# Performance work log

Measured on AMD Instinct MI355X. Metric: run time of the kernel, lower is better.

The kernel has to match this reference:

```python
import jax, jax.numpy as jnp
import numpy as np

N = 100000  # nodes
E = 1600000  # edges


def gcn_conv(x, W, b, src, dst, n_nodes):
    """PyG-style GCNConv: add self-loops, symmetric norm, linear, scatter-add, bias."""
    h = x @ W  # [N, F_out]
    loop = jnp.arange(n_nodes, dtype=src.dtype)
    s = jnp.concatenate([src, loop])  # source nodes (messages flow src -> dst)
    d = jnp.concatenate([dst, loop])
    deg = jax.ops.segment_sum(jnp.ones_like(d, dtype=h.dtype), d, num_segments=n_nodes)
    dinv = jnp.where(deg > 0, jax.lax.rsqrt(deg), 0.0)
    norm = dinv[s] * dinv[d]  # [E+N]
    msgs = h[s] * norm[:, None]  # [E+N, F_out] -- dominant memory traffic
    out = jax.ops.segment_sum(msgs, d, num_segments=n_nodes)
    return out + b


def setup_inputs() -> dict:
    key = jax.random.key(0)
    k1, k2, k3, k4 = jax.random.split(key, 4)
    x = jax.random.normal(k1, (N, 128), dtype=jnp.float32)
    edge_index = jax.random.randint(k2, (2, E), 0, N, dtype=jnp.int32)
    W1 = jax.random.normal(k3, (128, 64), dtype=jnp.float32) * (1.0 / np.sqrt(128))
    b1 = jnp.zeros((64,), dtype=jnp.float32)
    W2 = jax.random.normal(k4, (64, 16), dtype=jnp.float32) * (1.0 / np.sqrt(64))
    b2 = jnp.zeros((16,), dtype=jnp.float32)
    return {"x": x, "edge_index": edge_index, "W1": W1, "b1": b1, "W2": W2, "b2": b2}


def reference(x, edge_index, W1, b1, W2, b2):
    src, dst = edge_index[0], edge_index[1]
    h = gcn_conv(x, W1, b1, src, dst, N)
    h = jax.nn.leaky_relu(h, negative_slope=0.2)
    # dropout is identity in eval mode
    h = gcn_conv(h, W2, b2, src, dst, N)
    return jax.nn.log_softmax(h, axis=-1)
```

## Files before the change

### kernel.cpp

```cpp
#include <hip/hip_runtime.h>
#include <math.h>


#define CHUNK 4096
#define BSHIFT 9
#define BMASK 511
#define CAP 9216

typedef __bf16 bf16x8 __attribute__((ext_vector_type(8)));
typedef float f32x4 __attribute__((ext_vector_type(4)));

__device__ __forceinline__ unsigned f2b(float f) {
  unsigned u = __float_as_uint(f);
  return (u + 0x7FFF + ((u >> 16) & 1)) >> 16;
}

__global__ void binit_kernel(int* __restrict__ gbcursor, int nbc,
                             unsigned* __restrict__ h1s, int n) {
  int b = blockIdx.x * 256 + threadIdx.x;
  if (b < nbc) gbcursor[b] = b * CAP;
  if (blockIdx.x == 0 && threadIdx.x < 32) h1s[(size_t)n * 32 + threadIdx.x] = 0u;
}

__global__ __launch_bounds__(256) void scatterA_kernel(const int* __restrict__ src,
                                                       const int* __restrict__ dst,
                                                       int E, int nbc,
                                                       int* __restrict__ gbcursor,
                                                       int* __restrict__ tmp) {
  __shared__ int hist[256];
  __shared__ int segcur[256];
  int tid = threadIdx.x;
  int estart = blockIdx.x * CHUNK;
  int eend = min(E, estart + CHUNK);
  hist[tid] = 0;
  __syncthreads();
  for (int i = estart + tid; i < eend; i += 256)
    atomicAdd(&hist[dst[i] >> BSHIFT], 1);
  __syncthreads();
  if (tid < nbc) {
    int c = hist[tid];
    segcur[tid] = c ? atomicAdd(&gbcursor[tid], c) : 0;
  }
  __syncthreads();
  for (int i = estart + tid; i < eend; i += 256) {
    int d = dst[i];
    int b = d >> BSHIFT;
    int pos = atomicAdd(&segcur[b], 1);
    if (pos < (b + 1) * CAP)
      tmp[pos] = (src[i] << BSHIFT) | (d & BMASK);
  }
}

__global__ __launch_bounds__(1024) void csrbuild_kernel(const int* __restrict__ tmp,
                                                        const int* __restrict__ gbcursor,
                                                        int n, int* __restrict__ row_start,
                                                        int* __restrict__ degs,
                                                        float* __restrict__ dinv,
                                                        int* __restrict__ csr) {
  __shared__ int nh[512];
  __shared__ int sc[512];
  __shared__ int lcur[512];
  int b = blockIdx.x, tid = threadIdx.x;
  int base = b * CAP;
  int count = min(gbcursor[b] - base, CAP);
  if (tid < 512) nh[tid] = 0;
  __syncthreads();
  for (int i = tid; i < count; i += 1024) atomicAdd(&nh[tmp[base + i] & BMASK], 1);
  __syncthreads();
  int d = 0;
  if (tid < 512) { d = nh[tid]; sc[tid] = d; }
  __syncthreads();
  for (int off = 1; off < 512; off <<= 1) {
    int a = 0;
    if (tid < 512) { a = sc[tid]; if (tid >= off) a += sc[tid - off]; }
    __syncthreads();
    if (tid < 512) sc[tid] = a;
    __syncthreads();
  }
  if (tid < 512) {
    int e0 = base + sc[tid] - d;
    lcur[tid] = e0;
    int v = (b << BSHIFT) + tid;
    if (v < n) {
      row_start[v] = e0; degs[v] = d;
      dinv[v] = rsqrtf((float)(d + 1));
    }
  }
  __syncthreads();
  for (int i = tid; i < count; i += 1024) {
    int val = tmp[base + i];
    int pos = atomicAdd(&lcur[val & BMASK], 1);
    csr[pos] = val >> BSHIFT;
  }
}

__global__ __launch_bounds__(256, 4) void gemm1_kernel(const float* __restrict__ x,
                                                       const float* __restrict__ W1,
                                                       const float* __restrict__ dinv,
                                                       unsigned* __restrict__ h1s, int n) {
  __shared__ unsigned lds_u[64 * 68 * 2];
  unsigned* xs = lds_u;
  unsigned* wt = lds_u + 64 * 68;
  int tid = threadIdx.x;
  int vb = blockIdx.x * 64;
  int nrows = min(64, n - vb);

  const float4* xg = (const float4*)(x + (size_t)vb * 128);
#pragma unroll
  for (int it = 0; it < 8; ++it) {
    int idx = it * 256 + tid;
    int r = idx >> 5, c2 = idx & 31;
    float4 vv = make_float4(0.f, 0.f, 0.f, 0.f);
    if (r < nrows) vv = xg[idx];
    xs[r * 68 + c2 * 2] = (f2b(vv.y) << 16) | f2b(vv.x);
    xs[r * 68 + c2 * 2 + 1] = (f2b(vv.w) << 16) | f2b(vv.z);
  }
  unsigned short* wt16 = (unsigned short*)wt;
  const float4* wg = (const float4*)W1;
#pragma unroll
  for (int it = 0; it < 8; ++it) {
    int idx = it * 256 + tid;
    int k = idx >> 4, n0 = (idx & 15) * 4;
    float4 wv = wg[idx];
    wt16[(n0 + 0) * 136 + k] = (unsigned short)f2b(wv.x);
    wt16[(n0 + 1) * 136 + k] = (unsigned short)f2b(wv.y);
    wt16[(n0 + 2) * 136 + k] = (unsigned short)f2b(wv.z);
    wt16[(n0 + 3) * 136 + k] = (unsigned short)f2b(wv.w);
  }
  __syncthreads();

  int lane = tid & 63, wid = tid >> 6;
  int m16 = lane & 15, quad = lane >> 4;
  const unsigned* xp = xs + (wid * 16 + m16) * 68 + quad * 4;
  const unsigned* wp = wt + m16 * 68 + quad * 4;
  f32x4 acc[4] = {};
#pragma unroll
  for (int ks = 0; ks < 4; ++ks) {
    bf16x8 a = *(const bf16x8*)(xp + ks * 16);
#pragma unroll
    for (int nt = 0; nt < 4; ++nt) {
      bf16x8 b = *(const bf16x8*)(wp + nt * 16 * 68 + ks * 16);
      acc[nt] = __builtin_amdgcn_mfma_f32_16x16x32_bf16(a, b, acc[nt], 0, 0, 0);
    }
  }
  int rbase = vb + wid * 16 + quad * 4;
  float dvv[4];
#pragma unroll
  for (int reg = 0; reg < 4; ++reg) {
    int row = rbase + reg;
    dvv[reg] = (row < n) ? dinv[row] : 0.f;
  }
  unsigned short* h16 = (unsigned short*)h1s;
#pragma unroll
  for (int nt = 0; nt < 4; ++nt) {
    int col = nt * 16 + m16;
#pragma unroll
    for (int reg = 0; reg < 4; ++reg) {
      int row = rbase + reg;
      if (row < n)
        h16[(size_t)row * 64 + col] = (unsigned short)f2b(dvv[reg] * acc[nt][reg]);
    }
  }
}

struct f2 { float x, y; };
__device__ __forceinline__ void addu(f2& a, unsigned u) {
  a.x += __uint_as_float(u << 16);
  a.y += __uint_as_float(u);
}
__device__ __forceinline__ void addu4(f2* a, uint4 g) {
  addu(a[0], g.x); addu(a[1], g.y); addu(a[2], g.z); addu(a[3], g.w);
}

__global__ __launch_bounds__(256) void agg1_kernel(const uint4* __restrict__ h1s4,
                                                   const float* __restrict__ dinv,
                                                   const int* __restrict__ row_start,
                                                   const int* __restrict__ degs,
                                                   const int* __restrict__ csr,
                                                   const float* __restrict__ b1,
                                                   const float* __restrict__ W2,
                                                   unsigned* __restrict__ t, int n) {
  __shared__ float W2s[64 * 17];
  __shared__ float b1s[64];
  __shared__ float a_s[4][2][64];
  for (int i = threadIdx.x; i < 1024; i += 256)
    W2s[(i >> 4) * 17 + (i & 15)] = W2[i];
  if (threadIdx.x < 64) b1s[threadIdx.x] = b1[threadIdx.x];
  if (blockIdx.x == 0 && threadIdx.x < 8) t[(size_t)n * 8 + threadIdx.x] = 0u;
  __syncthreads();

  int wave = threadIdx.x >> 6, lane = threadIdx.x & 63;
  int half = lane >> 5, sub = lane & 31;
  int e = sub >> 3, c = sub & 7;
  int j = sub & 15, grp = (sub >> 4) & 1;

  for (int vbase = blockIdx.x * 8; vbase < n; vbase += gridDim.x * 8) {
    int v = vbase + wave * 2 + half;
    bool valid = (v < n);
    int vc = valid ? v : 0;
    int i = row_start[vc];
    int e1 = i + (valid ? degs[vc] : 0);
    float dv = valid ? dinv[vc] : 0.f;

    f2 a0[4];
#pragma unroll
    for (int k = 0; k < 4; ++k) a0[k] = {0.f, 0.f};
    {
      int s = (valid && sub < 8) ? v : n;
      addu4(a0, h1s4[(size_t)s * 8 + c]);
    }
    while (__any(i < e1)) {
      int i0 = i + e, i1 = i + 4 + e;
      int s0v = csr[i0];
      int s1v = csr[i1];
      int s0 = (i0 < e1) ? s0v : n;
      int s1 = (i1 < e1) ? s1v : n;
      uint4 g0 = h1s4[(size_t)s0 * 8 + c];
      uint4 g1 = h1s4[(size_t)s1 * 8 + c];
      addu4(a0, g0);
      addu4(a0, g1);
      i += 8;
    }
#pragma unroll
    for (int m = 8; m <= 16; m <<= 1) {
#pragma unroll
      for (int k = 0; k < 4; ++k) {
        a0[k].x += __shfl_xor(a0[k].x, m, 64);
        a0[k].y += __shfl_xor(a0[k].y, m, 64);
      }
    }
    if (sub < 8) {
#pragma unroll
      for (int k = 0; k < 4; ++k) {
        float z0 = fmaf(dv, a0[k].x, b1s[8 * sub + 2 * k]);
        float z1 = fmaf(dv, a0[k].y, b1s[8 * sub + 2 * k + 1]);
        a_s[wave][half][8 * sub + 2 * k] = fmaxf(z0, 0.2f * z0);
        a_s[wave][half][8 * sub + 2 * k + 1] = fmaxf(z1, 0.2f * z1);
      }
    }
    float p = 0.f;
#pragma unroll
    for (int q = 0; q < 16; ++q) {
      int f = grp * 16 + q;
      p = fmaf(a_s[wave][half][f], W2s[f * 17 + j], p);
    }
#pragma unroll
    for (int q = 0; q < 16; ++q) {
      int f = 32 + grp * 16 + q;
      p = fmaf(a_s[wave][half][f], W2s[f * 17 + j], p);
    }
    p += __shfl_xor(p, 16, 64);
    float pv = dv * p;
    float po = __shfl_xor(pv, 1, 64);
    if (valid && sub < 16 && !(sub & 1))
      t[(size_t)v * 8 + (sub >> 1)] = (f2b(po) << 16) | f2b(pv);
  }
}

__global__ __launch_bounds__(256) void agg2_kernel(const uint4* __restrict__ t4,
                                                   const float* __restrict__ dinv,
                                                   const int* __restrict__ row_start,
                                                   const int* __restrict__ degs,
                                                   const int* __restrict__ csr,
                                                   const float* __restrict__ b2,
                                                   float* __restrict__ out, int n) {
  int idx = blockIdx.x * 256 + threadIdx.x;
  int v = idx >> 4;
  if (v >= n) return;
  int sub = threadIdx.x & 15;
  int e = sub >> 1, c = sub & 1;
  float dv = dinv[v];
  int e0 = row_start[v], e1 = e0 + degs[v];
  f2 A0[4], A1[4];
#pragma unroll
  for (int k = 0; k < 4; ++k) { A0[k] = {0.f, 0.f}; A1[k] = {0.f, 0.f}; }
  {
    int s = (e == 0) ? v : n;
    addu4(A0, t4[(size_t)s * 2 + c]);
  }
  int i = e0;
  while (i + 8 < e1) {
    int i1 = i + 8 + e;
    int s0 = csr[i + e];
    int s1v = csr[i1];
    int s1 = (i1 < e1) ? s1v : n;
    uint4 g0 = t4[(size_t)s0 * 2 + c];
    uint4 g1 = t4[(size_t)s1 * 2 + c];
    addu4(A0, g0);
    addu4(A1, g1);
    i += 16;
  }
  if (i < e1) {
    int i0 = i + e;
    int sv = csr[i0];
    int s = (i0 < e1) ? sv : n;
    addu4(A0, t4[(size_t)s * 2 + c]);
  }
#pragma unroll
  for (int k = 0; k < 4; ++k) { A0[k].x += A1[k].x; A0[k].y += A1[k].y; }
#pragma unroll
  for (int m = 2; m <= 8; m <<= 1) {
#pragma unroll
    for (int k = 0; k < 4; ++k) {
      A0[k].x += __shfl_xor(A0[k].x, m, 64);
      A0[k].y += __shfl_xor(A0[k].y, m, 64);
    }
  }
  float4 bb0 = ((const float4*)b2)[c * 2];
  float4 bb1 = ((const float4*)b2)[c * 2 + 1];
  float z[8];
  z[0] = fmaf(dv, A0[0].x, bb0.x); z[1] = fmaf(dv, A0[0].y, bb0.y);
  z[2] = fmaf(dv, A0[1].x, bb0.z); z[3] = fmaf(dv, A0[1].y, bb0.w);
  z[4] = fmaf(dv, A0[2].x, bb1.x); z[5] = fmaf(dv, A0[2].y, bb1.y);
  z[6] = fmaf(dv, A0[3].x, bb1.z); z[7] = fmaf(dv, A0[3].y, bb1.w);
  float mx = z[0];
#pragma unroll
  for (int q = 1; q < 8; ++q) mx = fmaxf(mx, z[q]);
  mx = fmaxf(mx, __shfl_xor(mx, 1, 64));
  float ss = 0.f;
#pragma unroll
  for (int q = 0; q < 8; ++q) ss += expf(z[q] - mx);
  ss += __shfl_xor(ss, 1, 64);
  float lg = mx + logf(ss);
  if (e == 0) {
    float4 r0 = make_float4(z[0] - lg, z[1] - lg, z[2] - lg, z[3] - lg);
    float4 r1 = make_float4(z[4] - lg, z[5] - lg, z[6] - lg, z[7] - lg);
    float4* o = (float4*)out + (size_t)v * 4 + c * 2;
    o[0] = r0;
    o[1] = r1;
  }
}

extern "C" void kernel_launch(void* const* d_in, const int* in_sizes, int n_in,
                              void* d_out, int out_size, void* d_ws, size_t ws_size,
                              hipStream_t stream) {
  const float* x = (const float*)d_in[0];
  const int* edge_index = (const int*)d_in[1];
  const float* W1 = (const float*)d_in[2];
  const float* b1 = (const float*)d_in[3];
  const float* W2 = (const float*)d_in[4];
  const float* b2 = (const float*)d_in[5];
  float* out = (float*)d_out;

  int N_ = in_sizes[0] / 128;
  int E_ = in_sizes[1] / 2;
  const int* src = edge_index;
  const int* dst = edge_index + E_;
  int NBc = (N_ + BMASK) >> BSHIFT;

  char* ws = (char*)d_ws;
  size_t off = 0;
  auto take = [&](size_t bytes) {
    void* p = ws + off;
    off += (bytes + 255) & ~(size_t)255;
    return p;
  };
  unsigned* h1s = (unsigned*)take(((size_t)N_ + 1) * 32 * 4);
  size_t t_bytes = ((size_t)N_ + 1) * 8 * 4, tmp_bytes = (size_t)NBc * CAP * 4;
  void* t_union = take(t_bytes > tmp_bytes ? t_bytes : tmp_bytes);
  unsigned* t = (unsigned*)t_union;
  int* tmp = (int*)t_union;
  float* dinv = (float*)take((size_t)N_ * 4);
  int* degs = (int*)take((size_t)N_ * 4);
  int* row_start = (int*)take(((size_t)N_ + 1) * 4);
  int* csr = (int*)take(((size_t)NBc * CAP + 16) * 4);
  int* gbcursor = (int*)take((size_t)NBc * 4);
  (void)ws_size;

  binit_kernel<<<(NBc + 255) / 256, 256, 0, stream>>>(gbcursor, NBc, h1s, N_);
  scatterA_kernel<<<(E_ + CHUNK - 1) / CHUNK, 256, 0, stream>>>(src, dst, E_, NBc,
                                                                gbcursor, tmp);
  csrbuild_kernel<<<NBc, 1024, 0, stream>>>(tmp, gbcursor, N_, row_start, degs,
                                            dinv, csr);
  gemm1_kernel<<<(N_ + 63) / 64, 256, 0, stream>>>(x, W1, dinv, h1s, N_);
  agg1_kernel<<<2048, 256, 0, stream>>>((const uint4*)h1s, dinv, row_start, degs,
                                        csr, b1, W2, t, N_);
  agg2_kernel<<<(N_ * 16 + 255) / 256, 256, 0, stream>>>((const uint4*)t, dinv,
                                                         row_start, degs, csr,
                                                         b2, out, N_);
}
```

Baseline: 212.2 us.

## Replace bucketed CSR build with global atomic degree count, scan and scatter

Replaces the two-level bucketed CSR construction (LDS histograms per 512-node bucket) with a simpler pipeline: global atomic degree count, a two-pass block scan for row offsets, and a global atomic cursor scatter of source indices. It also prefetches the first 32 neighbour indices and gathers in both aggregation kernels to raise memory-level parallelism, and removes the dual accumulator in agg2. The simpler build adds more kernel launches and heavy global atomics on random destinations, which may cost more than the LDS-local bucketing it replaces. The scanC kernel has each thread sum up to about 100 block sums serially.

New measurement: 361.1 us. +70.2%, slower.

```diff
diff --git a/kernel.cpp b/kernel.cpp
--- a/kernel.cpp
+++ b/kernel.cpp
@@ -1,11 +1,6 @@
 #include <hip/hip_runtime.h>
 #include <math.h>
 
-
-#define CHUNK 4096
-#define BSHIFT 9
-#define BMASK 511
-#define CAP 9216
 
 typedef __bf16 bf16x8 __attribute__((ext_vector_type(8)));
 typedef float f32x4 __attribute__((ext_vector_type(4)));
@@ -15,82 +10,78 @@
   return (u + 0x7FFF + ((u >> 16) & 1)) >> 16;
 }
 
-__global__ void binit_kernel(int* __restrict__ gbcursor, int nbc,
-                             unsigned* __restrict__ h1s, int n) {
-  int b = blockIdx.x * 256 + threadIdx.x;
-  if (b < nbc) gbcursor[b] = b * CAP;
-  if (blockIdx.x == 0 && threadIdx.x < 32) h1s[(size_t)n * 32 + threadIdx.x] = 0u;
-}
-
-__global__ __launch_bounds__(256) void scatterA_kernel(const int* __restrict__ src,
-                                                       const int* __restrict__ dst,
-                                                       int E, int nbc,
-                                                       int* __restrict__ gbcursor,
-                                                       int* __restrict__ tmp) {
-  __shared__ int hist[256];
-  __shared__ int segcur[256];
+struct f2 { float x, y; };
+__device__ __forceinline__ void addu(f2& a, unsigned u) {
+  a.x += __uint_as_float(u << 16);
+  a.y += __uint_as_float(u & 0xffff0000u);
+}
+__device__ __forceinline__ void addu4(f2* a, uint4 g) {
+  addu(a[0], g.x); addu(a[1], g.y); addu(a[2], g.z); addu(a[3], g.w);
+}
+
+__global__ void zinit_kernel(int* __restrict__ deg, int n,
+                             unsigned* __restrict__ h1s, unsigned* __restrict__ t) {
+  for (int i = blockIdx.x * 256 + threadIdx.x; i < n; i += gridDim.x * 256) deg[i] = 0;
+  if (blockIdx.x == 0) {
+    if (threadIdx.x < 32) h1s[(size_t)n * 32 + threadIdx.x] = 0u;
+    else if (threadIdx.x < 40) t[(size_t)n * 8 + (threadIdx.x - 32)] = 0u;
+  }
+}
+
+__global__ __launch_bounds__(256) void degcount_kernel(const int* __restrict__ dst,
+                                                       int E, int* __restrict__ deg) {
+  int i = blockIdx.x * 256 + threadIdx.x;
+  if (i < E) atomicAdd(&deg[dst[i]], 1);
+}
+
+__global__ __launch_bounds__(1024) void scanA_kernel(const int* __restrict__ deg, int n,
+                                                     int* __restrict__ row_start,
+                                                     int* __restrict__ blocksum) {
+  __shared__ int sc[1024];
   int tid = threadIdx.x;
-  int estart = blockIdx.x * CHUNK;
-  int eend = min(E, estart + CHUNK);
-  hist[tid] = 0;
+  int v = blockIdx.x * 1024 + tid;
+  int d = (v < n) ? deg[v] : 0;
+  sc[tid] = d;
   __syncthreads();
-  for (int i = estart + tid; i < eend; i += 256)
-    atomicAdd(&hist[dst[i] >> BSHIFT], 1);
+  for (int off = 1; off < 1024; off <<= 1) {
+    int a = sc[tid];
+    int b = (tid >= off) ? sc[tid - off] : 0;
+    __syncthreads();
+    sc[tid] = a + b;
+    __syncthreads();
+  }
+  if (v < n) row_start[v] = sc[tid] - d;
+  if (tid == 1023) blocksum[blockIdx.x] = sc[1023];
+}
+
+__global__ __launch_bounds__(1024) void scanC_kernel(const int* __restrict__ deg, int n,
+                                                     int nb, const int* __restrict__ blocksum,
+                                                     int* __restrict__ row_start,
+                                                     int* __restrict__ cursor,
+                                                     float* __restrict__ dinv) {
+  __shared__ int bs[128];
+  int tid = threadIdx.x, b = blockIdx.x;
+  if (tid < nb) bs[tid] = blocksum[tid];
   __syncthreads();
-  if (tid < nbc) {
-    int c = hist[tid];
-    segcur[tid] = c ? atomicAdd(&gbcursor[tid], c) : 0;
-  }
-  __syncthreads();
-  for (int i = estart + tid; i < eend; i += 256) {
-    int d = dst[i];
-    int b = d >> BSHIFT;
-    int pos = atomicAdd(&segcur[b], 1);
-    if (pos < (b + 1) * CAP)
-      tmp[pos] = (src[i] << BSHIFT) | (d & BMASK);
-  }
-}
-
-__global__ __launch_bounds__(1024) void csrbuild_kernel(const int* __restrict__ tmp,
-                                                        const int* __restrict__ gbcursor,
-                                                        int n, int* __restrict__ row_start,
-                                                        int* __restrict__ degs,
-                                                        float* __restrict__ dinv,
-                                                        int* __restrict__ csr) {
-  __shared__ int nh[512];
-  __shared__ int sc[512];
-  __shared__ int lcur[512];
-  int b = blockIdx.x, tid = threadIdx.x;
-  int base = b * CAP;
-  int count = min(gbcursor[b] - base, CAP);
-  if (tid < 512) nh[tid] = 0;
-  __syncthreads();
-  for (int i = tid; i < count; i += 1024) atomicAdd(&nh[tmp[base + i] & BMASK], 1);
-  __syncthreads();
-  int d = 0;
-  if (tid < 512) { d = nh[tid]; sc[tid] = d; }
-  __syncthreads();
-  for (int off = 1; off < 512; off <<= 1) {
-    int a = 0;
-    if (tid < 512) { a = sc[tid]; if (tid >= off) a += sc[tid - off]; }
-    __syncthreads();
-    if (tid < 512) sc[tid] = a;
-    __syncthreads();
-  }
-  if (tid < 512) {
-    int e0 = base + sc[tid] - d;
-    lcur[tid] = e0;
-    int v = (b << BSHIFT) + tid;
-    if (v < n) {
-      row_start[v] = e0; degs[v] = d;
-      dinv[v] = rsqrtf((float)(d + 1));
-    }
-  }
-  __syncthreads();
-  for (int i = tid; i < count; i += 1024) {
-    int val = tmp[base + i];
-    int pos = atomicAdd(&lcur[val & BMASK], 1);
-    csr[pos] = val >> BSHIFT;
+  int off = 0;
+  for (int jj = 0; jj < b; ++jj) off += bs[jj];
+  int v = b * 1024 + tid;
+  if (v < n) {
+    int rs = row_start[v] + off;
+    row_start[v] = rs;
+    cursor[v] = rs;
+    dinv[v] = rsqrtf((float)(deg[v] + 1));
+  }
+}
+
+__global__ __launch_bounds__(256) void scatter_kernel(const int* __restrict__ src,
+                                                      const int* __restrict__ dst,
+                                                      int E, int* __restrict__ cursor,
+                                                      int* __restrict__ csr) {
+  int i = blockIdx.x * 256 + threadIdx.x;
+  if (i < E) {
+    int pos = atomicAdd(&cursor[dst[i]], 1);
+    csr[pos] = src[i];
   }
 }
 
@@ -161,15 +152,6 @@
         h16[(size_t)row * 64 + col] = (unsigned short)f2b(dvv[reg] * acc[nt][reg]);
     }
   }
-}
-
-struct f2 { float x, y; };
-__device__ __forceinline__ void addu(f2& a, unsigned u) {
-  a.x += __uint_as_float(u << 16);
-  a.y += __uint_as_float(u);
-}
-__device__ __forceinline__ void addu4(f2* a, uint4 g) {
-  addu(a[0], g.x); addu(a[1], g.y); addu(a[2], g.z); addu(a[3], g.w);
 }
 
 __global__ __launch_bounds__(256) void agg1_kernel(const uint4* __restrict__ h1s4,
@@ -186,7 +168,6 @@
   for (int i = threadIdx.x; i < 1024; i += 256)
     W2s[(i >> 4) * 17 + (i & 15)] = W2[i];
   if (threadIdx.x < 64) b1s[threadIdx.x] = b1[threadIdx.x];
-  if (blockIdx.x == 0 && threadIdx.x < 8) t[(size_t)n * 8 + threadIdx.x] = 0u;
   __syncthreads();
 
   int wave = threadIdx.x >> 6, lane = threadIdx.x & 63;
@@ -198,8 +179,9 @@
     int v = vbase + wave * 2 + half;
     bool valid = (v < n);
     int vc = valid ? v : 0;
-    int i = row_start[vc];
-    int e1 = i + (valid ? degs[vc] : 0);
+    int rs = row_start[vc];
+    int deg = valid ? degs[vc] : 0;
+    int e1 = rs + deg;
     float dv = valid ? dinv[vc] : 0.f;
 
     f2 a0[4];
@@ -209,16 +191,32 @@
       int s = (valid && sub < 8) ? v : n;
       addu4(a0, h1s4[(size_t)s * 8 + c]);
     }
+    int cv0[4], cv1[4];
+#pragma unroll
+    for (int it = 0; it < 4; ++it) {
+      cv0[it] = csr[rs + it * 8 + e];
+      cv1[it] = csr[rs + it * 8 + 4 + e];
+    }
+    uint4 g[8];
+#pragma unroll
+    for (int it = 0; it < 4; ++it) {
+      int k0 = rs + it * 8 + e, k1 = k0 + 4;
+      int s0 = (k0 < e1) ? cv0[it] : n;
+      int s1 = (k1 < e1) ? cv1[it] : n;
+      g[2 * it] = h1s4[(size_t)s0 * 8 + c];
+      g[2 * it + 1] = h1s4[(size_t)s1 * 8 + c];
+    }
+#pragma unroll
+    for (int k = 0; k < 8; ++k) addu4(a0, g[k]);
+    int i = rs + 32;
     while (__any(i < e1)) {
       int i0 = i + e, i1 = i + 4 + e;
       int s0v = csr[i0];
       int s1v = csr[i1];
       int s0 = (i0 < e1) ? s0v : n;
       int s1 = (i1 < e1) ? s1v : n;
-      uint4 g0 = h1s4[(size_t)s0 * 8 + c];
-      uint4 g1 = h1s4[(size_t)s1 * 8 + c];
-      addu4(a0, g0);
-      addu4(a0, g1);
+      addu4(a0, h1s4[(size_t)s0 * 8 + c]);
+      addu4(a0, h1s4[(size_t)s1 * 8 + c]);
       i += 8;
     }
 #pragma unroll
@@ -270,34 +268,34 @@
   int sub = threadIdx.x & 15;
   int e = sub >> 1, c = sub & 1;
   float dv = dinv[v];
-  int e0 = row_start[v], e1 = e0 + degs[v];
-  f2 A0[4], A1[4];
-#pragma unroll
-  for (int k = 0; k < 4; ++k) { A0[k] = {0.f, 0.f}; A1[k] = {0.f, 0.f}; }
+  int rs = row_start[v], e1 = rs + degs[v];
+  f2 A0[4];
+#pragma unroll
+  for (int k = 0; k < 4; ++k) A0[k] = {0.f, 0.f};
   {
     int s = (e == 0) ? v : n;
     addu4(A0, t4[(size_t)s * 2 + c]);
   }
-  int i = e0;
-  while (i + 8 < e1) {
-    int i1 = i + 8 + e;
-    int s0 = csr[i + e];
-    int s1v = csr[i1];
-    int s1 = (i1 < e1) ? s1v : n;
-    uint4 g0 = t4[(size_t)s0 * 2 + c];
-    uint4 g1 = t4[(size_t)s1 * 2 + c];
-    addu4(A0, g0);
-    addu4(A1, g1);
-    i += 16;
-  }
-  if (i < e1) {
+  int cv[4];
+#pragma unroll
+  for (int it = 0; it < 4; ++it) cv[it] = csr[rs + it * 8 + e];
+  uint4 g[4];
+#pragma unroll
+  for (int it = 0; it < 4; ++it) {
+    int k = rs + it * 8 + e;
+    int s = (k < e1) ? cv[it] : n;
+    g[it] = t4[(size_t)s * 2 + c];
+  }
+#pragma unroll
+  for (int k = 0; k < 4; ++k) addu4(A0, g[k]);
+  int i = rs + 32;
+  while (i < e1) {
     int i0 = i + e;
     int sv = csr[i0];
     int s = (i0 < e1) ? sv : n;
     addu4(A0, t4[(size_t)s * 2 + c]);
-  }
-#pragma unroll
-  for (int k = 0; k < 4; ++k) { A0[k].x += A1[k].x; A0[k].y += A1[k].y; }
+    i += 8;
+  }
 #pragma unroll
   for (int m = 2; m <= 8; m <<= 1) {
 #pragma unroll
@@ -346,7 +344,7 @@
   int E_ = in_sizes[1] / 2;
   const int* src = edge_index;
   const int* dst = edge_index + E_;
-  int NBc = (N_ + BMASK) >> BSHIFT;
+  int NBLK = (N_ + 1023) >> 10;
 
   char* ws = (char*)d_ws;
   size_t off = 0;
@@ -356,26 +354,25 @@
     return p;
   };
   unsigned* h1s = (unsigned*)take(((size_t)N_ + 1) * 32 * 4);
-  size_t t_bytes = ((size_t)N_ + 1) * 8 * 4, tmp_bytes = (size_t)NBc * CAP * 4;
-  void* t_union = take(t_bytes > tmp_bytes ? t_bytes : tmp_bytes);
-  unsigned* t = (unsigned*)t_union;
-  int* tmp = (int*)t_union;
+  unsigned* t = (unsigned*)take(((size_t)N_ + 1) * 8 * 4);
   float* dinv = (float*)take((size_t)N_ * 4);
-  int* degs = (int*)take((size_t)N_ * 4);
-  int* row_start = (int*)take(((size_t)N_ + 1) * 4);
-  int* csr = (int*)take(((size_t)NBc * CAP + 16) * 4);
-  int* gbcursor = (int*)take((size_t)NBc * 4);
+  int* deg = (int*)take((size_t)N_ * 4);
+  int* row_start = (int*)take((size_t)N_ * 4);
+  int* cursor = (int*)take((size_t)N_ * 4);
+  int* csr = (int*)take(((size_t)E_ + 64) * 4);
+  int* blocksum = (int*)take(128 * 4);
   (void)ws_size;
 
-  binit_kernel<<<(NBc + 255) / 256, 256, 0, stream>>>(gbcursor, NBc, h1s, N_);
-  scatterA_kernel<<<(E_ + CHUNK - 1) / CHUNK, 256, 0, stream>>>(src, dst, E_, NBc,
-                                                                gbcursor, tmp);
-  csrbuild_kernel<<<NBc, 1024, 0, stream>>>(tmp, gbcursor, N_, row_start, degs,
-                                            dinv, csr);
+  zinit_kernel<<<512, 256, 0, stream>>>(deg, N_, h1s, t);
+  degcount_kernel<<<(E_ + 255) / 256, 256, 0, stream>>>(dst, E_, deg);
+  scanA_kernel<<<NBLK, 1024, 0, stream>>>(deg, N_, row_start, blocksum);
+  scanC_kernel<<<NBLK, 1024, 0, stream>>>(deg, N_, NBLK, blocksum, row_start,
+                                          cursor, dinv);
+  scatter_kernel<<<(E_ + 255) / 256, 256, 0, stream>>>(src, dst, E_, cursor, csr);
   gemm1_kernel<<<(N_ + 63) / 64, 256, 0, stream>>>(x, W1, dinv, h1s, N_);
-  agg1_kernel<<<2048, 256, 0, stream>>>((const uint4*)h1s, dinv, row_start, degs,
+  agg1_kernel<<<2048, 256, 0, stream>>>((const uint4*)h1s, dinv, row_start, deg,
                                         csr, b1, W2, t, N_);
   agg2_kernel<<<(N_ * 16 + 255) / 256, 256, 0, stream>>>((const uint4*)t, dinv,
-                                                         row_start, degs, csr,
+                                                         row_start, deg, csr,
                                                          b2, out, N_);
 }
```
